# Kernel optimization log

Measured on AMD Instinct MI355X. Metric: run time of the kernel, lower is better.

## Reference

```python
import jax, jax.numpy as jnp
import numpy as np

B, T, D_IN, D_OUT = 8, 4096, 512, 512
STYLE, RANK, ALPHA = 256, 8, 1.0
NUM_LORA = (D_IN + D_OUT) * RANK


def setup_inputs() -> dict:
    key = jax.random.key(0)
    ks = jax.random.split(key, 8)
    s = 0.02
    return {
        "x": jax.random.normal(ks[0], (B, T, D_IN), jnp.float32),
        "style_emb": jax.random.normal(ks[1], (B, STYLE), jnp.float32),
        "w_base": jax.random.normal(ks[2], (D_OUT, D_IN), jnp.float32) * s,
        "b_base": jax.random.normal(ks[3], (D_OUT,), jnp.float32) * s,
        "w_h1": jax.random.normal(ks[4], (STYLE, STYLE), jnp.float32) * s,
        "b_h1": jax.random.normal(ks[5], (STYLE,), jnp.float32) * s,
        "w_h2": jax.random.normal(ks[6], (NUM_LORA, STYLE), jnp.float32) * s,
        "b_h2": jax.random.normal(ks[7], (NUM_LORA,), jnp.float32) * s,
    }


def reference(x, style_emb, w_base, b_base, w_h1, b_h1, w_h2, b_h2):
    # Base linear: [B,T,D_out]
    base_out = jnp.einsum("btd,od->bto", x, w_base) + b_base
    # Hypernet: Linear -> SiLU -> Linear producing per-sample LoRA params
    h = jax.nn.silu(style_emb @ w_h1.T + b_h1)          # [B, STYLE]
    raw = h @ w_h2.T + b_h2                             # [B, NUM_LORA]
    split = D_IN * RANK
    mat_a = raw[:, :split].reshape(B, RANK, D_IN)       # [B, r, D_in]
    mat_b = raw[:, split:].reshape(B, D_OUT, RANK)      # [B, D_out, r]
    # Low-rank path: x @ A^T @ B^T  (never materialize [B,D_out,D_in])
    down = jnp.einsum("btd,brd->btr", x, mat_a)         # [B, T, r]
    lora = jnp.einsum("btr,bor->bto", down, mat_b)      # [B, T, D_out]
    return base_out + ALPHA * lora
```

## Files before the change

### kernel.cpp

```cpp
#include <hip/hip_runtime.h>
#include <hip/hip_fp16.h>
#include <stdint.h>


#define NB 8
#define NT 4096
#define DIN 512
#define DOUT 512
#define NSTYLE 256
#define RANK 8
#define NLORA ((DIN + DOUT) * RANK)

typedef _Float16 f16x8 __attribute__((ext_vector_type(8)));
typedef float f32x4 __attribute__((ext_vector_type(4)));

__global__ void k_hyper1(const float* __restrict__ style,
                         const float* __restrict__ w_h1,
                         const float* __restrict__ b_h1,
                         float* __restrict__ h) {
  const int b = blockIdx.x;
  const int j = threadIdx.x;
  __shared__ float s[NSTYLE];
  s[j] = style[b * NSTYLE + j];
  __syncthreads();
  const float4* wrow = (const float4*)(w_h1 + (size_t)j * NSTYLE);
  float acc = b_h1[j];
#pragma unroll 8
  for (int k = 0; k < NSTYLE / 4; ++k) {
    float4 w4 = wrow[k];
    acc += s[4 * k + 0] * w4.x + s[4 * k + 1] * w4.y + s[4 * k + 2] * w4.z +
           s[4 * k + 3] * w4.w;
  }
  h[b * NSTYLE + j] = acc / (1.f + expf(-acc));
}

__global__ void k_hyper2(const float* __restrict__ h,
                         const float* __restrict__ w_h2,
                         const float* __restrict__ b_h2,
                         float* __restrict__ raw) {
  const int b = blockIdx.y;
  const int n = blockIdx.x * 256 + threadIdx.x;
  __shared__ float hs[NSTYLE];
  hs[threadIdx.x] = h[b * NSTYLE + threadIdx.x];
  __syncthreads();
  const float4* wrow = (const float4*)(w_h2 + (size_t)n * NSTYLE);
  float acc = b_h2[n];
#pragma unroll 8
  for (int k = 0; k < NSTYLE / 4; ++k) {
    float4 w4 = wrow[k];
    acc += hs[4 * k + 0] * w4.x + hs[4 * k + 1] * w4.y + hs[4 * k + 2] * w4.z +
           hs[4 * k + 3] * w4.w;
  }
  raw[(size_t)b * NLORA + n] = acc;
}

__global__ void k_weff(const float* __restrict__ raw,
                       const float* __restrict__ w_base,
                       _Float16* __restrict__ Wh) {
  const int oc = blockIdx.x;
  const int b = blockIdx.y;
  __shared__ float Als[RANK][DIN];
  __shared__ float Bls[16][RANK];
  const float* rb = raw + (size_t)b * NLORA;
  for (int i = threadIdx.x; i < RANK * DIN; i += 256)
    (&Als[0][0])[i] = rb[i];
  if (threadIdx.x < 16 * RANK) {
    int oo = threadIdx.x >> 3, r = threadIdx.x & 7;
    Bls[oo][r] = rb[DIN * RANK + (oc * 16 + oo) * RANK + r];
  }
  __syncthreads();
  for (int oo = 0; oo < 16; ++oo) {
    const int o = oc * 16 + oo;
    float br[RANK];
#pragma unroll
    for (int r = 0; r < RANK; ++r) br[r] = Bls[oo][r];
#pragma unroll
    for (int dd = 0; dd < DIN / 256; ++dd) {
      const int d = dd * 256 + threadIdx.x;
      float acc = w_base[(size_t)o * DIN + d];
#pragma unroll
      for (int r = 0; r < RANK; ++r) acc += br[r] * Als[r][d];
      Wh[((size_t)b * DOUT + o) * DIN + d] = (_Float16)acc;
    }
  }
}

#define BM 128
#define BN 128
#define BK 32

__global__ __launch_bounds__(256) void k_gemm(const float* __restrict__ x,
                                              const _Float16* __restrict__ Wh,
                                              const float* __restrict__ b_base,
                                              float* __restrict__ out) {
  const int nt = blockIdx.x;
  const int mt = blockIdx.y;
  const int b = blockIdx.z;

  __shared__ _Float16 Xs[BM][BK];
  __shared__ _Float16 Ws[BN][BK];

  const int tid = threadIdx.x;
  const int lane = tid & 63;
  const int wave = tid >> 6;
  const int wr = wave >> 1, wc = wave & 1;
  const int l16 = lane & 15, lq = lane >> 4;

  const float* xb = x + ((size_t)b * NT + (size_t)mt * BM) * DIN;
  const _Float16* wb = Wh + ((size_t)b * DOUT + (size_t)nt * BN) * DIN;

  f32x4 acc[4][4];
#pragma unroll
  for (int m = 0; m < 4; ++m)
#pragma unroll
    for (int n = 0; n < 4; ++n)
#pragma unroll
      for (int j = 0; j < 4; ++j) acc[m][n][j] = 0.f;

  const int xi = tid >> 1;
  const int xk = (tid & 1) * 16;
  const float* xsrc = xb + (size_t)xi * DIN + xk;

  for (int k0 = 0; k0 < DIN; k0 += BK) {
    __syncthreads();
    float4 f0 = *(const float4*)(xsrc + k0 + 0);
    float4 f1 = *(const float4*)(xsrc + k0 + 4);
    float4 f2 = *(const float4*)(xsrc + k0 + 8);
    float4 f3 = *(const float4*)(xsrc + k0 + 12);
    f16x8 h0, h1;
    h0[0] = (_Float16)f0.x; h0[1] = (_Float16)f0.y;
    h0[2] = (_Float16)f0.z; h0[3] = (_Float16)f0.w;
    h0[4] = (_Float16)f1.x; h0[5] = (_Float16)f1.y;
    h0[6] = (_Float16)f1.z; h0[7] = (_Float16)f1.w;
    h1[0] = (_Float16)f2.x; h1[1] = (_Float16)f2.y;
    h1[2] = (_Float16)f2.z; h1[3] = (_Float16)f2.w;
    h1[4] = (_Float16)f3.x; h1[5] = (_Float16)f3.y;
    h1[6] = (_Float16)f3.z; h1[7] = (_Float16)f3.w;
    *(f16x8*)&Xs[xi][xk] = h0;
    *(f16x8*)&Xs[xi][xk + 8] = h1;
#pragma unroll
    for (int i = 0; i < 2; ++i) {
      const int c = i * 256 + wave * 64 + lane;
      const int jr = c >> 2;
      const int kc = (c & 3) * 8;
      const _Float16* g = wb + (size_t)jr * DIN + k0 + kc;
      __builtin_amdgcn_global_load_lds(
          (const __attribute__((address_space(1))) void*)g,
          (__attribute__((address_space(3))) void*)((char*)&Ws[0][0] +
                                                    i * 4096 + wave * 1024),
          16, 0, 0);
    }
    __syncthreads();
    f16x8 af[4], bf[4];
#pragma unroll
    for (int m = 0; m < 4; ++m)
      af[m] = *(const f16x8*)&Xs[wr * 64 + m * 16 + l16][lq * 8];
#pragma unroll
    for (int n = 0; n < 4; ++n)
      bf[n] = *(const f16x8*)&Ws[wc * 64 + n * 16 + l16][lq * 8];
#pragma unroll
    for (int m = 0; m < 4; ++m)
#pragma unroll
      for (int n = 0; n < 4; ++n)
        acc[m][n] = __builtin_amdgcn_mfma_f32_16x16x32_f16(af[m], bf[n],
                                                           acc[m][n], 0, 0, 0);
  }

  float bv[4];
#pragma unroll
  for (int n = 0; n < 4; ++n)
    bv[n] = b_base[nt * BN + wc * 64 + n * 16 + l16];

#pragma unroll
  for (int m = 0; m < 4; ++m) {
#pragma unroll
    for (int j = 0; j < 4; ++j) {
      const int r = mt * BM + wr * 64 + m * 16 + lq * 4 + j;
      float* orow = out + ((size_t)b * NT + r) * DOUT + nt * BN;
#pragma unroll
      for (int n = 0; n < 4; ++n)
        orow[wc * 64 + n * 16 + l16] = acc[m][n][j] + bv[n];
    }
  }
}

extern "C" void kernel_launch(void* const* d_in, const int* in_sizes, int n_in,
                              void* d_out, int out_size, void* d_ws,
                              size_t ws_size, hipStream_t stream) {
  const float* x = (const float*)d_in[0];
  const float* style = (const float*)d_in[1];
  const float* w_base = (const float*)d_in[2];
  const float* b_base = (const float*)d_in[3];
  const float* w_h1 = (const float*)d_in[4];
  const float* b_h1 = (const float*)d_in[5];
  const float* w_h2 = (const float*)d_in[6];
  const float* b_h2 = (const float*)d_in[7];
  float* out = (float*)d_out;

  char* ws = (char*)d_ws;
  float* h = (float*)ws;
  float* raw = (float*)(ws + 8192);
  _Float16* Wh = (_Float16*)(ws + 8192 + 262144);

  k_hyper1<<<NB, NSTYLE, 0, stream>>>(style, w_h1, b_h1, h);
  k_hyper2<<<dim3(NLORA / 256, NB), 256, 0, stream>>>(h, w_h2, b_h2, raw);
  k_weff<<<dim3(DOUT / 16, NB), 256, 0, stream>>>(raw, w_base, Wh);
  k_gemm<<<dim3(DOUT / BN, NT / BM, NB), 256, 0, stream>>>(x, Wh, b_base, out);
}
```

Measured before the change: 199.8 us.

## Restructure hypernet, pre-swizzle effective weights, and stream full-N GEMM tiles

```diff
diff --git a/kernel.cpp b/kernel.cpp
--- a/kernel.cpp
+++ b/kernel.cpp
@@ -34,152 +34,177 @@
   h[b * NSTYLE + j] = acc / (1.f + expf(-acc));
 }
 
-__global__ void k_hyper2(const float* __restrict__ h,
-                         const float* __restrict__ w_h2,
-                         const float* __restrict__ b_h2,
-                         float* __restrict__ raw) {
-  const int b = blockIdx.y;
-  const int n = blockIdx.x * 256 + threadIdx.x;
-  __shared__ float hs[NSTYLE];
-  hs[threadIdx.x] = h[b * NSTYLE + threadIdx.x];
-  __syncthreads();
-  const float4* wrow = (const float4*)(w_h2 + (size_t)n * NSTYLE);
-  float acc = b_h2[n];
-#pragma unroll 8
-  for (int k = 0; k < NSTYLE / 4; ++k) {
-    float4 w4 = wrow[k];
-    acc += hs[4 * k + 0] * w4.x + hs[4 * k + 1] * w4.y + hs[4 * k + 2] * w4.z +
-           hs[4 * k + 3] * w4.w;
-  }
-  raw[(size_t)b * NLORA + n] = acc;
+__global__ __launch_bounds__(256) void k_hyper2(const float* __restrict__ h,
+                                                const float* __restrict__ w_h2,
+                                                const float* __restrict__ b_h2,
+                                                float* __restrict__ raw) {
+  __shared__ float hs[NB * NSTYLE];
+  const int t = threadIdx.x;
+#pragma unroll
+  for (int i = 0; i < NB * NSTYLE / 256; ++i) hs[i * 256 + t] = h[i * 256 + t];
+  __syncthreads();
+  const int w = t >> 6, lane = t & 63;
+  const int n = blockIdx.x * 4 + w;
+  float4 w4 = *(const float4*)(w_h2 + (size_t)n * NSTYLE + lane * 4);
+  float acc[NB];
+#pragma unroll
+  for (int b = 0; b < NB; ++b) {
+    float4 hb = *(const float4*)(&hs[b * NSTYLE + lane * 4]);
+    acc[b] = hb.x * w4.x + hb.y * w4.y + hb.z * w4.z + hb.w * w4.w;
+#pragma unroll
+    for (int m = 32; m > 0; m >>= 1) acc[b] += __shfl_xor(acc[b], m);
+  }
+  if (lane == 0) {
+    const float bb = b_h2[n];
+#pragma unroll
+    for (int b = 0; b < NB; ++b) raw[(size_t)b * NLORA + n] = acc[b] + bb;
+  }
 }
 
 __global__ void k_weff(const float* __restrict__ raw,
                        const float* __restrict__ w_base,
-                       _Float16* __restrict__ Wh) {
-  const int oc = blockIdx.x;
+                       _Float16* __restrict__ Whf) {
+  const int cg = blockIdx.x;
   const int b = blockIdx.y;
-  __shared__ float Als[RANK][DIN];
+  const int t = threadIdx.x;
+  __shared__ float Als[RANK * DIN];
+  __shared__ float Wbs[16 * 516];
   __shared__ float Bls[16][RANK];
   const float* rb = raw + (size_t)b * NLORA;
-  for (int i = threadIdx.x; i < RANK * DIN; i += 256)
-    (&Als[0][0])[i] = rb[i];
-  if (threadIdx.x < 16 * RANK) {
-    int oo = threadIdx.x >> 3, r = threadIdx.x & 7;
-    Bls[oo][r] = rb[DIN * RANK + (oc * 16 + oo) * RANK + r];
-  }
-  __syncthreads();
-  for (int oo = 0; oo < 16; ++oo) {
-    const int o = oc * 16 + oo;
-    float br[RANK];
-#pragma unroll
-    for (int r = 0; r < RANK; ++r) br[r] = Bls[oo][r];
-#pragma unroll
-    for (int dd = 0; dd < DIN / 256; ++dd) {
-      const int d = dd * 256 + threadIdx.x;
-      float acc = w_base[(size_t)o * DIN + d];
-#pragma unroll
-      for (int r = 0; r < RANK; ++r) acc += br[r] * Als[r][d];
-      Wh[((size_t)b * DOUT + o) * DIN + d] = (_Float16)acc;
-    }
-  }
-}
-
-#define BM 128
-#define BN 128
-#define BK 32
-
-__global__ __launch_bounds__(256) void k_gemm(const float* __restrict__ x,
-                                              const _Float16* __restrict__ Wh,
-                                              const float* __restrict__ b_base,
-                                              float* __restrict__ out) {
-  const int nt = blockIdx.x;
-  const int mt = blockIdx.y;
-  const int b = blockIdx.z;
-
-  __shared__ _Float16 Xs[BM][BK];
-  __shared__ _Float16 Ws[BN][BK];
-
-  const int tid = threadIdx.x;
-  const int lane = tid & 63;
-  const int wave = tid >> 6;
-  const int wr = wave >> 1, wc = wave & 1;
+#pragma unroll
+  for (int i = 0; i < 4; ++i)
+    *(float4*)(&Als[(i * 256 + t) * 4]) = *(const float4*)(&rb[(i * 256 + t) * 4]);
+#pragma unroll
+  for (int i = 0; i < 8; ++i) {
+    int fi = i * 256 + t;
+    int oo = fi >> 7, d4 = fi & 127;
+    float4 v = *(const float4*)(&w_base[((size_t)(cg * 16 + oo)) * DIN + d4 * 4]);
+    *(float4*)(&Wbs[oo * 516 + d4 * 4]) = v;
+  }
+  if (t < 16 * RANK) {
+    int oo = t >> 3, r = t & 7;
+    Bls[oo][r] = rb[DIN * RANK + (cg * 16 + oo) * RANK + r];
+  }
+  __syncthreads();
+  const int lane = t & 63;
+  const int oo = lane & 15;
+  const int koff = ((lane >> 4) & 3) * 8;
+  float br[RANK];
+#pragma unroll
+  for (int r = 0; r < RANK; ++r) br[r] = Bls[oo][r];
+  _Float16* dst = Whf + (size_t)b * (DOUT * DIN) + cg * 8192;
+#pragma unroll
+  for (int i = 0; i < 4; ++i) {
+    const int q = i * 256 + t;
+    const int kkg = q >> 6;
+    const int kb = kkg * 32 + koff;
+    f16x8 v;
+#pragma unroll
+    for (int j = 0; j < 8; ++j) {
+      float a = Wbs[oo * 516 + kb + j];
+#pragma unroll
+      for (int r = 0; r < RANK; ++r) a += br[r] * Als[r * DIN + kb + j];
+      v[j] = (_Float16)a;
+    }
+    *(f16x8*)(dst + (size_t)q * 8) = v;
+  }
+}
+
+#define BM 32
+#define BK 64
+
+__global__ __launch_bounds__(256, 3) void k_gemm(
+    const float* __restrict__ x, const _Float16* __restrict__ Whf,
+    const float* __restrict__ b_base, float* __restrict__ out) {
+  const int id = blockIdx.x;
+  const int b = id & 7;
+  const int mt = id >> 3;
+  const int t = threadIdx.x;
+  const int lane = t & 63;
+  const int w = t >> 6;
   const int l16 = lane & 15, lq = lane >> 4;
 
+  __shared__ _Float16 Xs[2][BM * BK];
+
   const float* xb = x + ((size_t)b * NT + (size_t)mt * BM) * DIN;
-  const _Float16* wb = Wh + ((size_t)b * DOUT + (size_t)nt * BN) * DIN;
-
-  f32x4 acc[4][4];
-#pragma unroll
-  for (int m = 0; m < 4; ++m)
-#pragma unroll
-    for (int n = 0; n < 4; ++n)
+  const _Float16* wb = Whf + (size_t)b * (DOUT * DIN) + (size_t)(w * 8) * 8192 +
+                       (size_t)lane * 8;
+
+  f32x4 acc[2][8];
+#pragma unroll
+  for (int m = 0; m < 2; ++m)
+#pragma unroll
+    for (int n = 0; n < 8; ++n)
 #pragma unroll
       for (int j = 0; j < 4; ++j) acc[m][n][j] = 0.f;
 
-  const int xi = tid >> 1;
-  const int xk = (tid & 1) * 16;
-  const float* xsrc = xb + (size_t)xi * DIN + xk;
-
-  for (int k0 = 0; k0 < DIN; k0 += BK) {
+  const int srow = t >> 3, sc = t & 7;
+  const float* xsrc = xb + (size_t)srow * DIN + sc * 8;
+  const int swz_w = (srow * 128 + sc * 16) ^ ((srow & 7) << 4);
+
+  {
+    float4 f0 = *(const float4*)(xsrc + 0);
+    float4 f1 = *(const float4*)(xsrc + 4);
+    f16x8 hh;
+    hh[0] = (_Float16)f0.x; hh[1] = (_Float16)f0.y;
+    hh[2] = (_Float16)f0.z; hh[3] = (_Float16)f0.w;
+    hh[4] = (_Float16)f1.x; hh[5] = (_Float16)f1.y;
+    hh[6] = (_Float16)f1.z; hh[7] = (_Float16)f1.w;
+    *(f16x8*)((char*)&Xs[0][0] + swz_w) = hh;
+  }
+  __syncthreads();
+
+  for (int step = 0; step < DIN / BK; ++step) {
+    const int cur = step & 1;
+    float4 f0p, f1p;
+    if (step < DIN / BK - 1) {
+      f0p = *(const float4*)(xsrc + (step + 1) * BK + 0);
+      f1p = *(const float4*)(xsrc + (step + 1) * BK + 4);
+    }
+#pragma unroll
+    for (int kk = 0; kk < 2; ++kk) {
+      const int kkg = step * 2 + kk;
+      f16x8 af[2], bf[8];
+#pragma unroll
+      for (int m = 0; m < 2; ++m) {
+        const int row = m * 16 + l16;
+        const int byte = (row * 128 + (kk * 4 + lq) * 16) ^ ((row & 7) << 4);
+        af[m] = *(const f16x8*)((const char*)&Xs[cur][0] + byte);
+      }
+#pragma unroll
+      for (int n = 0; n < 8; ++n)
+        bf[n] = *(const f16x8*)(wb + (size_t)n * 8192 + (size_t)kkg * 512);
+#pragma unroll
+      for (int m = 0; m < 2; ++m)
+#pragma unroll
+        for (int n = 0; n < 8; ++n)
+          acc[m][n] = __builtin_amdgcn_mfma_f32_16x16x32_f16(af[m], bf[n],
+                                                             acc[m][n], 0, 0, 0);
+    }
+    if (step < DIN / BK - 1) {
+      f16x8 hh;
+      hh[0] = (_Float16)f0p.x; hh[1] = (_Float16)f0p.y;
+      hh[2] = (_Float16)f0p.z; hh[3] = (_Float16)f0p.w;
+      hh[4] = (_Float16)f1p.x; hh[5] = (_Float16)f1p.y;
+      hh[6] = (_Float16)f1p.z; hh[7] = (_Float16)f1p.w;
+      *(f16x8*)((char*)&Xs[cur ^ 1][0] + swz_w) = hh;
+    }
     __syncthreads();
-    float4 f0 = *(const float4*)(xsrc + k0 + 0);
-    float4 f1 = *(const float4*)(xsrc + k0 + 4);
-    float4 f2 = *(const float4*)(xsrc + k0 + 8);
-    float4 f3 = *(const float4*)(xsrc + k0 + 12);
-    f16x8 h0, h1;
-    h0[0] = (_Float16)f0.x; h0[1] = (_Float16)f0.y;
-    h0[2] = (_Float16)f0.z; h0[3] = (_Float16)f0.w;
-    h0[4] = (_Float16)f1.x; h0[5] = (_Float16)f1.y;
-    h0[6] = (_Float16)f1.z; h0[7] = (_Float16)f1.w;
-    h1[0] = (_Float16)f2.x; h1[1] = (_Float16)f2.y;
-    h1[2] = (_Float16)f2.z; h1[3] = (_Float16)f2.w;
-    h1[4] = (_Float16)f3.x; h1[5] = (_Float16)f3.y;
-    h1[6] = (_Float16)f3.z; h1[7] = (_Float16)f3.w;
-    *(f16x8*)&Xs[xi][xk] = h0;
-    *(f16x8*)&Xs[xi][xk + 8] = h1;
-#pragma unroll
-    for (int i = 0; i < 2; ++i) {
-      const int c = i * 256 + wave * 64 + lane;
-      const int jr = c >> 2;
-      const int kc = (c & 3) * 8;
-      const _Float16* g = wb + (size_t)jr * DIN + k0 + kc;
-      __builtin_amdgcn_global_load_lds(
-          (const __attribute__((address_space(1))) void*)g,
-          (__attribute__((address_space(3))) void*)((char*)&Ws[0][0] +
-                                                    i * 4096 + wave * 1024),
-          16, 0, 0);
-    }
-    __syncthreads();
-    f16x8 af[4], bf[4];
-#pragma unroll
-    for (int m = 0; m < 4; ++m)
-      af[m] = *(const f16x8*)&Xs[wr * 64 + m * 16 + l16][lq * 8];
-#pragma unroll
-    for (int n = 0; n < 4; ++n)
-      bf[n] = *(const f16x8*)&Ws[wc * 64 + n * 16 + l16][lq * 8];
-#pragma unroll
-    for (int m = 0; m < 4; ++m)
-#pragma unroll
-      for (int n = 0; n < 4; ++n)
-        acc[m][n] = __builtin_amdgcn_mfma_f32_16x16x32_f16(af[m], bf[n],
-                                                           acc[m][n], 0, 0, 0);
-  }
-
-  float bv[4];
-#pragma unroll
-  for (int n = 0; n < 4; ++n)
-    bv[n] = b_base[nt * BN + wc * 64 + n * 16 + l16];
-
-#pragma unroll
-  for (int m = 0; m < 4; ++m) {
+  }
+
+  float bv[8];
+#pragma unroll
+  for (int n = 0; n < 8; ++n) bv[n] = b_base[w * 128 + n * 16 + l16];
+
+#pragma unroll
+  for (int m = 0; m < 2; ++m) {
 #pragma unroll
     for (int j = 0; j < 4; ++j) {
-      const int r = mt * BM + wr * 64 + m * 16 + lq * 4 + j;
-      float* orow = out + ((size_t)b * NT + r) * DOUT + nt * BN;
-#pragma unroll
-      for (int n = 0; n < 4; ++n)
-        orow[wc * 64 + n * 16 + l16] = acc[m][n][j] + bv[n];
+      const int r = mt * BM + m * 16 + lq * 4 + j;
+      float* orow = out + ((size_t)b * NT + r) * DOUT;
+#pragma unroll
+      for (int n = 0; n < 8; ++n)
+        orow[w * 128 + n * 16 + l16] = acc[m][n][j] + bv[n];
     }
   }
 }
@@ -200,10 +225,10 @@
   char* ws = (char*)d_ws;
   float* h = (float*)ws;
   float* raw = (float*)(ws + 8192);
-  _Float16* Wh = (_Float16*)(ws + 8192 + 262144);
+  _Float16* Whf = (_Float16*)(ws + 8192 + 262144);
 
   k_hyper1<<<NB, NSTYLE, 0, stream>>>(style, w_h1, b_h1, h);
-  k_hyper2<<<dim3(NLORA / 256, NB), 256, 0, stream>>>(h, w_h2, b_h2, raw);
-  k_weff<<<dim3(DOUT / 16, NB), 256, 0, stream>>>(raw, w_base, Wh);
-  k_gemm<<<dim3(DOUT / BN, NT / BM, NB), 256, 0, stream>>>(x, Wh, b_base, out);
-}
+  k_hyper2<<<NLORA / 4, 256, 0, stream>>>(h, w_h2, b_h2, raw);
+  k_weff<<<dim3(DOUT / 16, NB), 256, 0, stream>>>(raw, w_base, Whf);
+  k_gemm<<<(NT / BM) * NB, 256, 0, stream>>>(x, Whf, b_base, out);
+}
```

After: 184.1 us. -7.8%, faster.
